# Kernel optimization log

Hardware: AMD Instinct MI355X
Metric: run time of the kernel (lower is better)

The kernel has to match this reference:

```python
import jax, jax.numpy as jnp
import numpy as np

HOPS = 4
ALPHA = 0.1
N = 100000   # nodes
E = 1600000  # edges (before self loops)
DX = 128     # x feature dim
DY = 32      # y (soft label) dim


def setup_inputs() -> dict:
    key = jax.random.key(0)
    k1, k2, k3, k4 = jax.random.split(key, 4)
    x = jax.random.normal(k1, (N, DX), dtype=jnp.float32)
    y = jax.random.normal(k2, (N, DY), dtype=jnp.float32)
    src = jax.random.randint(k3, (E,), 0, N)
    dst = jax.random.randint(k4, (E,), 0, N)
    # emulate remove_self_loops with static shapes: perturb any accidental self loop
    dst = jnp.where(src == dst, (dst + 1) % N, dst)
    edge_index = jnp.stack([src, dst]).astype(jnp.int64)
    return {"x": x, "y": y, "edge_index": edge_index}


def reference(x, y, edge_index):
    src, dst = edge_index[0], edge_index[1]
    # add_self_loops (edge_index already has self loops removed)
    loop = jnp.arange(N, dtype=src.dtype)
    src = jnp.concatenate([src, loop])
    dst = jnp.concatenate([dst, loop])
    # symmetric normalization: w_e = deg(src)^-1/2 * deg(dst)^-1/2, deg counted on dst
    deg = jax.ops.segment_sum(jnp.ones_like(dst, dtype=x.dtype), dst, num_segments=N)
    dinv = jnp.where(deg > 0, deg ** -0.5, 0.0)
    w = dinv[src] * dinv[dst]  # [E+N]

    def spmm(v):
        # adj[src, dst] = w  =>  (adj @ v)[i] = sum_{e: src_e = i} w_e * v[dst_e]
        return jax.ops.segment_sum(w[:, None] * v[dst], src, num_segments=N)

    for _ in range(HOPS):
        x_prime = spmm(x)
        y_prime = spmm(y)
        if ALPHA > 0:
            x_prime = (1.0 - ALPHA) * x_prime + ALPHA * x
            y_prime = (1.0 - ALPHA) * y_prime + ALPHA * y
        x, y = x_prime, y_prime
    return x, y
```

## Files before the change

kernel.cpp:

```cpp
#include <hip/hip_runtime.h>


#define NN 100000
#define EE 1600000
#define NPAD 100096
#define NBKT 391
#define CAP 1024

#define GETREG_XCC_IMM (((32 - 1) << 11) | (0 << 6) | 20)

__device__ __forceinline__ float bflo(unsigned w) { return __uint_as_float(w << 16); }
__device__ __forceinline__ float bfhi(unsigned w) { return __uint_as_float(w & 0xffff0000u); }
__device__ __forceinline__ unsigned packbf(float a, float b) {
    unsigned ua = __float_as_uint(a), ub = __float_as_uint(b);
    unsigned ra = (ua + 0x7fffu + ((ua >> 16) & 1u)) >> 16;
    unsigned rb = (ub + 0x7fffu + ((ub >> 16) & 1u)) >> 16;
    return ra | (rb << 16);
}


__global__ void detect_kernel(const int* __restrict__ raw, int* __restrict__ flag) {
    if (threadIdx.x == 0 && blockIdx.x == 0) {
        int is64 = 1;
        for (int k = 1; k < 16; k += 2) {
            if (raw[k] != 0) { is64 = 0; break; }
        }
        *flag = is64;
    }
}

__global__ void zero_kernel(int* __restrict__ bufs, int total) {
    int i = blockIdx.x * blockDim.x + threadIdx.x;
    if (i < total) bufs[i] = 0;
}

__global__ void passA_kernel(const void* __restrict__ raw, const int* __restrict__ flag,
                             int* __restrict__ indeg_rep, int* __restrict__ bcur,
                             int* __restrict__ buf) {
    int e = blockIdx.x * blockDim.x + threadIdx.x;
    int r = __builtin_amdgcn_s_getreg(GETREG_XCC_IMM) & 7;
    if (e < EE) {
        int s, d;
        if (*flag) {
            s = (int)((const long long*)raw)[e];
            d = (int)((const long long*)raw)[EE + e];
        } else {
            s = ((const int*)raw)[e];
            d = ((const int*)raw)[EE + e];
        }
        atomicAdd(&indeg_rep[r * NPAD + d], 1);
        int b = s >> 8;
        int pos = atomicAdd(&bcur[r * 512 + b], 1);
        if (pos < CAP)
            buf[((size_t)(r * NBKT + b)) * CAP + pos] = ((s & 255) << 17) | d;
    }
}

__global__ void bucket_scan_kernel(const int* __restrict__ bcur, int* __restrict__ bucket_base,
                                   int* __restrict__ rowptr) {
    __shared__ int s[512];
    int tid = threadIdx.x;
    int v = 0;
    if (tid < NBKT) {
        #pragma unroll
        for (int r = 0; r < 8; ++r) {
            int c = bcur[r * 512 + tid];
            v += (c < CAP) ? c : CAP;
        }
    }
    s[tid] = v;
    __syncthreads();
    for (int off = 1; off < 512; off <<= 1) {
        int t = (tid >= off) ? s[tid - off] : 0;
        __syncthreads();
        s[tid] += t;
        __syncthreads();
    }
    if (tid < NBKT) bucket_base[tid] = s[tid] - v;
    if (tid == 0) rowptr[NN] = EE;
}

__global__ void dinv_kernel(const int* __restrict__ indeg_rep, float* __restrict__ dinv) {
    int i = blockIdx.x * blockDim.x + threadIdx.x;
    if (i < NN) {
        int ind = 1;
        #pragma unroll
        for (int r = 0; r < 8; ++r) ind += indeg_rep[r * NPAD + i];
        dinv[i] = rsqrtf((float)ind);
    }
}

__global__ void cast_kernel(const float4* __restrict__ x0, const float4* __restrict__ y0,
                            const float* __restrict__ dinv, uint4* __restrict__ zx,
                            uint4* __restrict__ zy) {
    int t = blockIdx.x * blockDim.x + threadIdx.x;
    if (t < NN * 16) {
        int node = t >> 4, c = t & 15;
        float di = dinv[node];
        float4 a = x0[(size_t)node * 32 + c * 2];
        float4 b = x0[(size_t)node * 32 + c * 2 + 1];
        uint4 o;
        o.x = packbf(di * a.x, di * a.y); o.y = packbf(di * a.z, di * a.w);
        o.z = packbf(di * b.x, di * b.y); o.w = packbf(di * b.z, di * b.w);
        zx[(size_t)node * 16 + c] = o;
    } else if (t < NN * 20) {
        int u = t - NN * 16;
        int node = u >> 2, c = u & 3;
        float di = dinv[node];
        float4 a = y0[(size_t)node * 8 + c * 2];
        float4 b = y0[(size_t)node * 8 + c * 2 + 1];
        uint4 o;
        o.x = packbf(di * a.x, di * a.y); o.y = packbf(di * a.z, di * a.w);
        o.z = packbf(di * b.x, di * b.y); o.w = packbf(di * b.z, di * b.w);
        zy[(size_t)node * 4 + c] = o;
    }
}

__global__ __launch_bounds__(256) void passB_kernel(const int* __restrict__ bcur,
                                                    const int* __restrict__ buf,
                                                    const int* __restrict__ bucket_base,
                                                    int* __restrict__ rowptr,
                                                    int* __restrict__ dst_sorted) {
    int b = blockIdx.x;
    int tid = threadIdx.x;
    __shared__ int cnt[8], off[9];
    __shared__ int edges[8 * CAP];
    __shared__ int hist[256];
    __shared__ int sc[256];
    __shared__ int base_s;

    if (tid < 8) {
        int c = bcur[tid * 512 + b];
        cnt[tid] = (c < CAP) ? c : CAP;
    }
    hist[tid] = 0;
    __syncthreads();
    if (tid == 0) {
        int run = 0;
        #pragma unroll
        for (int r = 0; r < 8; ++r) { off[r] = run; run += cnt[r]; }
        off[8] = run;
        base_s = bucket_base[b];
    }
    __syncthreads();
    #pragma unroll
    for (int r = 0; r < 8; ++r) {
        int c = cnt[r];
        const int* src = buf + ((size_t)(r * NBKT + b)) * CAP;
        for (int i = tid; i < c; i += 256) edges[off[r] + i] = src[i];
    }
    __syncthreads();
    int total = off[8];
    for (int i = tid; i < total; i += 256) atomicAdd(&hist[edges[i] >> 17], 1);
    __syncthreads();
    int hv = hist[tid];
    sc[tid] = hv;
    __syncthreads();
    for (int o = 1; o < 256; o <<= 1) {
        int t = (tid >= o) ? sc[tid - o] : 0;
        __syncthreads();
        sc[tid] += t;
        __syncthreads();
    }
    int excl = sc[tid] - hv;
    int node = (b << 8) + tid;
    if (node < NN) rowptr[node] = base_s + excl;
    hist[tid] = excl;
    __syncthreads();
    for (int i = tid; i < total; i += 256) {
        int p = edges[i];
        int pos = atomicAdd(&hist[p >> 17], 1);
        dst_sorted[base_s + pos] = p & 0x1ffff;
    }
}

template <bool OUTBF>
__global__ __launch_bounds__(256) void hop_kernel(const int* __restrict__ rowptr,
                                                  const int* __restrict__ dst_sorted,
                                                  const float* __restrict__ dinv,
                                                  const uint4* __restrict__ zx,
                                                  const uint4* __restrict__ zy,
                                                  void* __restrict__ nx,
                                                  void* __restrict__ ny) {
    int t = blockIdx.x * blockDim.x + threadIdx.x;
    int row = t >> 6, lane = t & 63;
    if (row >= NN) return;
    int beg = rowptr[row], end = rowptr[row + 1];

    int g = lane >> 4, sub = lane & 15;
    float ax[8] = {0.f, 0.f, 0.f, 0.f, 0.f, 0.f, 0.f, 0.f};
    for (int e = beg + g; e < end; e += 4) {
        int d = dst_sorted[e];
        uint4 w = zx[(size_t)d * 16 + sub];
        ax[0] += bflo(w.x); ax[1] += bfhi(w.x);
        ax[2] += bflo(w.y); ax[3] += bfhi(w.y);
        ax[4] += bflo(w.z); ax[5] += bfhi(w.z);
        ax[6] += bflo(w.w); ax[7] += bfhi(w.w);
    }
    #pragma unroll
    for (int m = 16; m <= 32; m <<= 1) {
        #pragma unroll
        for (int i = 0; i < 8; ++i) ax[i] += __shfl_xor(ax[i], m);
    }

    int gy = lane >> 2, sy = lane & 3;
    float ay[8] = {0.f, 0.f, 0.f, 0.f, 0.f, 0.f, 0.f, 0.f};
    for (int e = beg + gy; e < end; e += 16) {
        int d = dst_sorted[e];
        uint4 w = zy[(size_t)d * 4 + sy];
        ay[0] += bflo(w.x); ay[1] += bfhi(w.x);
        ay[2] += bflo(w.y); ay[3] += bfhi(w.y);
        ay[4] += bflo(w.z); ay[5] += bfhi(w.z);
        ay[6] += bflo(w.w); ay[7] += bfhi(w.w);
    }
    #pragma unroll
    for (int m = 4; m <= 32; m <<= 1) {
        #pragma unroll
        for (int i = 0; i < 8; ++i) ay[i] += __shfl_xor(ay[i], m);
    }

    float di = dinv[row];
    float sg = 0.9f * di;
    float sl = 0.9f * di + 0.1f / di;

    if (g == 0) {
        uint4 wz = zx[(size_t)row * 16 + sub];
        float c[8] = { bflo(wz.x), bfhi(wz.x), bflo(wz.y), bfhi(wz.y),
                       bflo(wz.z), bfhi(wz.z), bflo(wz.w), bfhi(wz.w) };
        float r[8];
        #pragma unroll
        for (int i = 0; i < 8; ++i) r[i] = sg * ax[i] + sl * c[i];
        if constexpr (OUTBF) {
            uint4 o;
            o.x = packbf(di * r[0], di * r[1]); o.y = packbf(di * r[2], di * r[3]);
            o.z = packbf(di * r[4], di * r[5]); o.w = packbf(di * r[6], di * r[7]);
            ((uint4*)nx)[(size_t)row * 16 + sub] = o;
        } else {
            float4 a, b;
            a.x = r[0]; a.y = r[1]; a.z = r[2]; a.w = r[3];
            b.x = r[4]; b.y = r[5]; b.z = r[6]; b.w = r[7];
            ((float4*)nx)[(size_t)row * 32 + sub * 2]     = a;
            ((float4*)nx)[(size_t)row * 32 + sub * 2 + 1] = b;
        }
    }
    if (gy == 0) {
        uint4 wz = zy[(size_t)row * 4 + sy];
        float c[8] = { bflo(wz.x), bfhi(wz.x), bflo(wz.y), bfhi(wz.y),
                       bflo(wz.z), bfhi(wz.z), bflo(wz.w), bfhi(wz.w) };
        float r[8];
        #pragma unroll
        for (int i = 0; i < 8; ++i) r[i] = sg * ay[i] + sl * c[i];
        if constexpr (OUTBF) {
            uint4 o;
            o.x = packbf(di * r[0], di * r[1]); o.y = packbf(di * r[2], di * r[3]);
            o.z = packbf(di * r[4], di * r[5]); o.w = packbf(di * r[6], di * r[7]);
            ((uint4*)ny)[(size_t)row * 4 + sy] = o;
        } else {
            float4 a, b;
            a.x = r[0]; a.y = r[1]; a.z = r[2]; a.w = r[3];
            b.x = r[4]; b.y = r[5]; b.z = r[6]; b.w = r[7];
            ((float4*)ny)[(size_t)row * 8 + sy * 2]     = a;
            ((float4*)ny)[(size_t)row * 8 + sy * 2 + 1] = b;
        }
    }
}

extern "C" void kernel_launch(void* const* d_in, const int* in_sizes, int n_in,
                              void* d_out, int out_size, void* d_ws, size_t ws_size,
                              hipStream_t stream) {
    const float* x0  = (const float*)d_in[0];
    const float* y0  = (const float*)d_in[1];
    const void*  raw = d_in[2];

    float* out_x = (float*)d_out;
    float* out_y = out_x + (size_t)NN * 128;

    int*   flag        = (int*)d_ws;
    int*   indeg_rep   = flag + 16;
    int*   bcur        = indeg_rep + 8 * NPAD;
    int*   bucket_base = bcur + 4096;
    int*   rowptr      = bucket_base + 512;
    float* dinv        = (float*)(rowptr + 100112);
    int*   buf         = (int*)(dinv + NPAD);
    int*   dst_sorted  = buf + (size_t)8 * NBKT * CAP;
    uint4* zxA         = (uint4*)(dst_sorted + EE);
    uint4* zxB         = zxA + (size_t)NN * 16;
    uint4* zyA         = (uint4*)(zxB + (size_t)NN * 16);
    uint4* zyB         = zyA + (size_t)NN * 4;

    const int B = 256;
    const int GW = (NN * 64 + B - 1) / B;
    const int ZTOT = 8 * NPAD + 4096;

    detect_kernel<<<1, 64, 0, stream>>>((const int*)raw, flag);
    zero_kernel<<<(ZTOT + B - 1) / B, B, 0, stream>>>(indeg_rep, ZTOT);
    passA_kernel<<<(EE + B - 1) / B, B, 0, stream>>>(raw, flag, indeg_rep, bcur, buf);
    bucket_scan_kernel<<<1, 512, 0, stream>>>(bcur, bucket_base, rowptr);
    dinv_kernel<<<(NN + B - 1) / B, B, 0, stream>>>(indeg_rep, dinv);
    cast_kernel<<<(NN * 20 + B - 1) / B, B, 0, stream>>>(
        (const float4*)x0, (const float4*)y0, dinv, zxA, zyA);
    passB_kernel<<<NBKT, 256, 0, stream>>>(bcur, buf, bucket_base, rowptr, dst_sorted);

    hop_kernel<true><<<GW, B, 0, stream>>>(rowptr, dst_sorted, dinv, zxA, zyA, zxB, zyB);
    hop_kernel<true><<<GW, B, 0, stream>>>(rowptr, dst_sorted, dinv, zxB, zyB, zxA, zyA);
    hop_kernel<true><<<GW, B, 0, stream>>>(rowptr, dst_sorted, dinv, zxA, zyA, zxB, zyB);
    hop_kernel<false><<<GW, B, 0, stream>>>(rowptr, dst_sorted, dinv, zxB, zyB, out_x, out_y);
}
```

Measured before the change: 676.7 us.

## Bucket edges via block-local shared-memory sort with one global atomic per bucket

The edge-bucketing pass now gives each block a chunk of 4096 edges. The block builds a shared-memory histogram over source buckets, sorts its edges locally, reserves space with one global atomic per bucket, and writes contiguous runs into a single per-bucket buffer. This replaces the per-edge global atomics on per-XCC bucket counters and the 8 replicated buffers, which also simplifies the gather in passB. In exchange, passA uses much more shared memory and launches fewer blocks. The padded counters limit false sharing, and the per-bucket capacity of 5120 may overflow on skewed inputs.

```diff
diff --git a/kernel.cpp b/kernel.cpp
--- a/kernel.cpp
+++ b/kernel.cpp
@@ -5,7 +5,8 @@
 #define EE 1600000
 #define NPAD 100096
 #define NBKT 391
-#define CAP 1024
+#define CHUNK 4096
+#define CAP2 5120
 
 #define GETREG_XCC_IMM (((32 - 1) << 11) | (0 << 6) | 20)
 
@@ -34,14 +35,33 @@
     if (i < total) bufs[i] = 0;
 }
 
-__global__ void passA_kernel(const void* __restrict__ raw, const int* __restrict__ flag,
-                             int* __restrict__ indeg_rep, int* __restrict__ bcur,
-                             int* __restrict__ buf) {
-    int e = blockIdx.x * blockDim.x + threadIdx.x;
+__global__ __launch_bounds__(256) void passA_kernel(const void* __restrict__ raw,
+                                                    const int* __restrict__ flag,
+                                                    int* __restrict__ indeg_rep,
+                                                    int* __restrict__ gbcur,
+                                                    int* __restrict__ buf) {
+    __shared__ unsigned short sh_b[CHUNK];
+    __shared__ unsigned int   sh_p[CHUNK];
+    __shared__ unsigned int   sh_sorted[CHUNK];
+    __shared__ unsigned short sh_bs[CHUNK];
+    __shared__ int hist[512];
+    __shared__ int excl[512];
+    __shared__ int gbase[512];
+    __shared__ int lcur[512];
+
+    int tid = threadIdx.x;
+    int base = blockIdx.x * CHUNK;
+    int nval = EE - base; if (nval > CHUNK) nval = CHUNK;
     int r = __builtin_amdgcn_s_getreg(GETREG_XCC_IMM) & 7;
-    if (e < EE) {
+    int is64 = *flag;
+
+    hist[tid] = 0; hist[tid + 256] = 0;
+    __syncthreads();
+
+    for (int i = tid; i < nval; i += 256) {
+        int e = base + i;
         int s, d;
-        if (*flag) {
+        if (is64) {
             s = (int)((const long long*)raw)[e];
             d = (int)((const long long*)raw)[EE + e];
         } else {
@@ -50,23 +70,57 @@
         }
         atomicAdd(&indeg_rep[r * NPAD + d], 1);
         int b = s >> 8;
-        int pos = atomicAdd(&bcur[r * 512 + b], 1);
-        if (pos < CAP)
-            buf[((size_t)(r * NBKT + b)) * CAP + pos] = ((s & 255) << 17) | d;
-    }
-}
-
-__global__ void bucket_scan_kernel(const int* __restrict__ bcur, int* __restrict__ bucket_base,
+        sh_b[i] = (unsigned short)b;
+        sh_p[i] = ((unsigned)(s & 255) << 17) | (unsigned)d;
+        atomicAdd(&hist[b], 1);
+    }
+    __syncthreads();
+
+    excl[tid] = hist[tid];
+    excl[tid + 256] = hist[tid + 256];
+    __syncthreads();
+    for (int off = 1; off < 512; off <<= 1) {
+        int a0 = (tid >= off) ? excl[tid - off] : 0;
+        int a1 = (tid + 256 >= off) ? excl[tid + 256 - off] : 0;
+        __syncthreads();
+        excl[tid] += a0;
+        excl[tid + 256] += a1;
+        __syncthreads();
+    }
+    int inc0 = excl[tid], inc1 = excl[tid + 256];
+    int h0 = hist[tid],  h1 = hist[tid + 256];
+    __syncthreads();
+    int e0 = inc0 - h0, e1 = inc1 - h1;
+    excl[tid] = e0; excl[tid + 256] = e1;
+    lcur[tid] = e0; lcur[tid + 256] = e1;
+    if (h0 > 0) gbase[tid]       = atomicAdd(&gbcur[tid * 16], h0);
+    if (h1 > 0) gbase[tid + 256] = atomicAdd(&gbcur[(tid + 256) * 16], h1);
+    __syncthreads();
+
+    for (int i = tid; i < nval; i += 256) {
+        int b = sh_b[i];
+        int pos = atomicAdd(&lcur[b], 1);
+        sh_sorted[pos] = sh_p[i];
+        sh_bs[pos] = (unsigned short)b;
+    }
+    __syncthreads();
+
+    for (int i = tid; i < nval; i += 256) {
+        int b = sh_bs[i];
+        int gpos = gbase[b] + (i - excl[b]);
+        if (gpos < CAP2)
+            buf[(size_t)b * CAP2 + gpos] = (int)sh_sorted[i];
+    }
+}
+
+__global__ void bucket_scan_kernel(const int* __restrict__ gbcur, int* __restrict__ bucket_base,
                                    int* __restrict__ rowptr) {
     __shared__ int s[512];
     int tid = threadIdx.x;
     int v = 0;
     if (tid < NBKT) {
-        #pragma unroll
-        for (int r = 0; r < 8; ++r) {
-            int c = bcur[r * 512 + tid];
-            v += (c < CAP) ? c : CAP;
-        }
+        int c = gbcur[tid * 16];
+        v = (c < CAP2) ? c : CAP2;
     }
     s[tid] = v;
     __syncthreads();
@@ -116,42 +170,32 @@
     }
 }
 
-__global__ __launch_bounds__(256) void passB_kernel(const int* __restrict__ bcur,
+__global__ __launch_bounds__(256) void passB_kernel(const int* __restrict__ gbcur,
                                                     const int* __restrict__ buf,
                                                     const int* __restrict__ bucket_base,
                                                     int* __restrict__ rowptr,
                                                     int* __restrict__ dst_sorted) {
     int b = blockIdx.x;
     int tid = threadIdx.x;
-    __shared__ int cnt[8], off[9];
-    __shared__ int edges[8 * CAP];
+    __shared__ int edges[CAP2];
     __shared__ int hist[256];
     __shared__ int sc[256];
-    __shared__ int base_s;
-
-    if (tid < 8) {
-        int c = bcur[tid * 512 + b];
-        cnt[tid] = (c < CAP) ? c : CAP;
+    __shared__ int base_s, tot_s;
+
+    if (tid == 0) {
+        int c = gbcur[b * 16];
+        tot_s = (c < CAP2) ? c : CAP2;
+        base_s = bucket_base[b];
     }
     hist[tid] = 0;
     __syncthreads();
-    if (tid == 0) {
-        int run = 0;
-        #pragma unroll
-        for (int r = 0; r < 8; ++r) { off[r] = run; run += cnt[r]; }
-        off[8] = run;
-        base_s = bucket_base[b];
-    }
-    __syncthreads();
-    #pragma unroll
-    for (int r = 0; r < 8; ++r) {
-        int c = cnt[r];
-        const int* src = buf + ((size_t)(r * NBKT + b)) * CAP;
-        for (int i = tid; i < c; i += 256) edges[off[r] + i] = src[i];
-    }
-    __syncthreads();
-    int total = off[8];
-    for (int i = tid; i < total; i += 256) atomicAdd(&hist[edges[i] >> 17], 1);
+    int total = tot_s;
+    const int* src = buf + (size_t)b * CAP2;
+    for (int i = tid; i < total; i += 256) {
+        int p = src[i];
+        edges[i] = p;
+        atomicAdd(&hist[p >> 17], 1);
+    }
     __syncthreads();
     int hv = hist[tid];
     sc[tid] = hv;
@@ -277,12 +321,12 @@
 
     int*   flag        = (int*)d_ws;
     int*   indeg_rep   = flag + 16;
-    int*   bcur        = indeg_rep + 8 * NPAD;
-    int*   bucket_base = bcur + 4096;
+    int*   gbcur       = indeg_rep + 8 * NPAD;
+    int*   bucket_base = gbcur + 512 * 16;
     int*   rowptr      = bucket_base + 512;
     float* dinv        = (float*)(rowptr + 100112);
     int*   buf         = (int*)(dinv + NPAD);
-    int*   dst_sorted  = buf + (size_t)8 * NBKT * CAP;
+    int*   dst_sorted  = buf + (size_t)NBKT * CAP2;
     uint4* zxA         = (uint4*)(dst_sorted + EE);
     uint4* zxB         = zxA + (size_t)NN * 16;
     uint4* zyA         = (uint4*)(zxB + (size_t)NN * 16);
@@ -290,16 +334,16 @@
 
     const int B = 256;
     const int GW = (NN * 64 + B - 1) / B;
-    const int ZTOT = 8 * NPAD + 4096;
+    const int ZTOT = 8 * NPAD + 512 * 16;
 
     detect_kernel<<<1, 64, 0, stream>>>((const int*)raw, flag);
     zero_kernel<<<(ZTOT + B - 1) / B, B, 0, stream>>>(indeg_rep, ZTOT);
-    passA_kernel<<<(EE + B - 1) / B, B, 0, stream>>>(raw, flag, indeg_rep, bcur, buf);
-    bucket_scan_kernel<<<1, 512, 0, stream>>>(bcur, bucket_base, rowptr);
+    passA_kernel<<<(EE + CHUNK - 1) / CHUNK, 256, 0, stream>>>(raw, flag, indeg_rep, gbcur, buf);
+    bucket_scan_kernel<<<1, 512, 0, stream>>>(gbcur, bucket_base, rowptr);
     dinv_kernel<<<(NN + B - 1) / B, B, 0, stream>>>(indeg_rep, dinv);
     cast_kernel<<<(NN * 20 + B - 1) / B, B, 0, stream>>>(
         (const float4*)x0, (const float4*)y0, dinv, zxA, zyA);
-    passB_kernel<<<NBKT, 256, 0, stream>>>(bcur, buf, bucket_base, rowptr, dst_sorted);
+    passB_kernel<<<NBKT, 256, 0, stream>>>(gbcur, buf, bucket_base, rowptr, dst_sorted);
 
     hop_kernel<true><<<GW, B, 0, stream>>>(rowptr, dst_sorted, dinv, zxA, zyA, zxB, zyB);
     hop_kernel<true><<<GW, B, 0, stream>>>(rowptr, dst_sorted, dinv, zxB, zyB, zxA, zyA);
```

Result: faster. 615.4 us (-9.1%).
